# Kernel optimization log

Hardware: AMD Instinct MI355X
Metric: run time of the kernel (lower is better)

Reference implementation:

```python
import jax, jax.numpy as jnp
import numpy as np

B, S, E = 4, 2048, 1024
H, D = 16, 64  # num_heads, head_size; H*D == E


def setup_inputs() -> dict:
    key = jax.random.key(0)
    ks = jax.random.split(key, 6)
    scale = E ** -0.5
    x = jax.random.normal(ks[0], (B, S, E), dtype=jnp.float32)
    # per-head bias-free q/k/v projections, stacked over heads: [H, E, D]
    Wq = jax.random.normal(ks[1], (H, E, D), dtype=jnp.float32) * scale
    Wk = jax.random.normal(ks[2], (H, E, D), dtype=jnp.float32) * scale
    Wv = jax.random.normal(ks[3], (H, E, D), dtype=jnp.float32) * scale
    # output projection: Linear(H*D, E) with bias
    Wproj = jax.random.normal(ks[4], (H * D, E), dtype=jnp.float32) * ((H * D) ** -0.5)
    bproj = jax.random.normal(ks[5], (E,), dtype=jnp.float32) * 0.01
    return {"x": x, "Wq": Wq, "Wk": Wk, "Wv": Wv, "Wproj": Wproj, "bproj": bproj}


def reference(x, Wq, Wk, Wv, Wproj, bproj):
    # Batched equivalent of the per-head loop: each head h computes
    # q = x @ Wq[h], k = x @ Wk[h], v = x @ Wv[h]
    q = jnp.einsum("bse,hed->bhsd", x, Wq)
    k = jnp.einsum("bse,hed->bhsd", x, Wk)
    v = jnp.einsum("bse,hed->bhsd", x, Wv)
    # causal scaled dot-product attention, scale = head_size**-0.5
    scores = jnp.einsum("bhqd,bhkd->bhqk", q, k) * (D ** -0.5)
    causal = jnp.tril(jnp.ones((S, S), dtype=bool))  # [S, S]
    scores = jnp.where(causal, scores, jnp.finfo(scores.dtype).min)
    attn = jax.nn.softmax(scores, axis=-1)  # dropout = identity in eval
    out = jnp.einsum("bhqk,bhkd->bhqd", attn, v)
    # concat heads along the feature dim, then project (dropout = identity)
    out = out.transpose(0, 2, 1, 3).reshape(B, S, H * D)
    return out @ Wproj + bproj
```

## Files before the change

kernel.cpp:

```cpp
#include <hip/hip_runtime.h>
#include <stdint.h>

typedef unsigned short u16;
typedef __attribute__((ext_vector_type(8))) short bf16x8;
typedef __attribute__((ext_vector_type(8))) unsigned short u16x8;
typedef __attribute__((ext_vector_type(4))) float f32x4;

#define S_LEN 2048
#define EDIM 1024
#define NH 16
#define HD 64

static __device__ __forceinline__ u16 f2bf(float f) {
  union { float f; uint32_t u; } v; v.f = f;
  uint32_t r = v.u + 0x7fffu + ((v.u >> 16) & 1u);
  return (u16)(r >> 16);
}

static __device__ __forceinline__ void gload_lds16(const u16* g, u16* l) {
  __builtin_amdgcn_global_load_lds(
      (const __attribute__((address_space(1))) void*)g,
      (__attribute__((address_space(3))) void*)l, 16, 0, 0);
}

static __device__ __forceinline__ bf16x8 gload16(const u16* p) {
  bf16x8 r;
  asm volatile("global_load_dwordx4 %0, %1, off" : "=v"(r) : "v"(p));
  return r;
}

#define WAIT_VM(n)                                   \
  do {                                               \
    asm volatile("s_waitcnt vmcnt(" #n ")");         \
    __builtin_amdgcn_sched_barrier(0);               \
  } while (0)

#define BARRIER()                                    \
  do {                                               \
    __builtin_amdgcn_s_barrier();                    \
    __builtin_amdgcn_sched_barrier(0);               \
  } while (0)

__global__ __launch_bounds__(256) void pack_inputs(
    const float* __restrict__ x, const float* __restrict__ Wq,
    const float* __restrict__ Wk, const float* __restrict__ Wv,
    const float* __restrict__ Wp,
    u16* __restrict__ xb, u16* __restrict__ wqkvT, u16* __restrict__ wprojT) {
  const int blk = blockIdx.x;
  const int tid = threadIdx.x;
  if (blk < 8192) {
    int idx = blk * 256 + tid;
    float4 v = ((const float4*)x)[idx];
    ushort4 o;
    o.x = f2bf(v.x); o.y = f2bf(v.y); o.z = f2bf(v.z); o.w = f2bf(v.w);
    ((ushort4*)xb)[idx] = o;
    return;
  }
  __shared__ u16 tile[64][65];
  const float* src;
  size_t src_rs;
  u16* dst;
  if (blk < 8960) {
    int t = blk - 8192;
    int mh = t >> 4;
    int et = t & 15;
    int m = mh >> 4, h = mh & 15;
    const float* W = (m == 0) ? Wq : (m == 1) ? Wk : Wv;
    src = W + ((size_t)(h * EDIM + et * 64)) * HD;
    src_rs = HD;
    dst = wqkvT + (size_t)(m * 1024 + h * 64) * 1024 + et * 64;
  } else {
    int t = blk - 8960;
    int kt = t >> 4, nt = t & 15;
    src = Wp + (size_t)(kt * 64) * 1024 + nt * 64;
    src_rs = 1024;
    dst = wprojT + (size_t)(nt * 64) * 1024 + kt * 64;
  }
  {
    const int rr = tid >> 4;
    const int c4 = (tid & 15) << 2;
#pragma unroll
    for (int p = 0; p < 4; p++) {
      const int r = p * 16 + rr;
      float4 v = *(const float4*)(src + (size_t)r * src_rs + c4);
      tile[r][c4 + 0] = f2bf(v.x);
      tile[r][c4 + 1] = f2bf(v.y);
      tile[r][c4 + 2] = f2bf(v.z);
      tile[r][c4 + 3] = f2bf(v.w);
    }
  }
  __syncthreads();
  {
    const int rr = tid >> 3;
    const int c8 = (tid & 7) << 3;
#pragma unroll
    for (int p = 0; p < 2; p++) {
      const int r = p * 32 + rr;
      u16x8 o;
#pragma unroll
      for (int j = 0; j < 8; j++) o[j] = tile[c8 + j][r];
      *(u16x8*)(dst + (size_t)r * 1024 + c8) = o;
    }
  }
}

template <int EPI>
__global__ __launch_bounds__(256) void gemm128(
    const u16* __restrict__ A, const u16* __restrict__ Bt,
    const float* __restrict__ bias,
    u16* __restrict__ o0, u16* __restrict__ o1, u16* __restrict__ o2,
    float* __restrict__ of, int K, int N) {
  __shared__ __align__(16) u16 As[128 * 64];
  __shared__ __align__(16) u16 Bs[128 * 64];
  const int tid  = threadIdx.x;
  const int lane = tid & 63;
  const int wave = tid >> 6;
  const int wm = wave >> 1;
  const int wn = wave & 1;
  const int col = lane & 15;
  const int quad = lane >> 4;
  const int cs = col & 7;
  const int m0 = blockIdx.y << 7;
  const int n0 = blockIdx.x << 7;

  const int srow  = lane >> 3;
  const int sslot = (lane & 7) ^ srow;
  const u16* gA = A + (size_t)(m0 + (wave << 5) + srow) * K + sslot * 8;
  const u16* gB = Bt + (size_t)(n0 + (wave << 5) + srow) * K + sslot * 8;
  u16* lA = &As[(wave << 5) << 6];
  u16* lB = &Bs[(wave << 5) << 6];

  f32x4 acc[4][4];
#pragma unroll
  for (int i = 0; i < 4; i++)
#pragma unroll
    for (int j = 0; j < 4; j++) acc[i][j] = (f32x4){0.f, 0.f, 0.f, 0.f};

  for (int kk = 0; kk < K; kk += 64) {
    __syncthreads();
#pragma unroll
    for (int i = 0; i < 4; i++) {
      gload_lds16(gA + (size_t)(i * 8) * K + kk, lA + i * 512);
      gload_lds16(gB + (size_t)(i * 8) * K + kk, lB + i * 512);
    }
    __syncthreads();

#pragma unroll
    for (int x = 0; x < 2; x++) {
      bf16x8 af[4], bfr[4];
#pragma unroll
      for (int i = 0; i < 4; i++)
        af[i] = *(const bf16x8*)(
            &As[((wm * 64 + i * 16 + col) << 6) + ((((x << 2) + quad) ^ cs) << 3)]);
#pragma unroll
      for (int j = 0; j < 4; j++)
        bfr[j] = *(const bf16x8*)(
            &Bs[((wn * 64 + j * 16 + col) << 6) + ((((x << 2) + quad) ^ cs) << 3)]);
#pragma unroll
      for (int i = 0; i < 4; i++)
#pragma unroll
        for (int j = 0; j < 4; j++)
          acc[i][j] = __builtin_amdgcn_mfma_f32_16x16x32_bf16(af[i], bfr[j],
                                                              acc[i][j], 0, 0, 0);
    }
  }

#pragma unroll
  for (int i = 0; i < 4; i++) {
#pragma unroll
    for (int j = 0; j < 4; j++) {
      const int rg0 = m0 + wm * 64 + i * 16 + quad * 4;
      const int cg = n0 + wn * 64 + j * 16 + col;
      if (EPI == 0) {
        const int mat = cg >> 10;
        const int rem = cg & 1023;
        const int h = rem >> 6;
        const int d = rem & 63;
        const int b = rg0 >> 11;
        const int s0 = rg0 & 2047;
        if (mat == 2) {
          ushort4 o;
          o.x = f2bf(acc[i][j][0]); o.y = f2bf(acc[i][j][1]);
          o.z = f2bf(acc[i][j][2]); o.w = f2bf(acc[i][j][3]);
          *(ushort4*)(&o2[(((size_t)(b * NH + h) * HD + d) << 11) + s0]) = o;
        } else {
          u16* dst = (mat == 0) ? o0 : o1;
#pragma unroll
          for (int r = 0; r < 4; r++)
            dst[((size_t)((b * NH + h) * S_LEN + s0 + r) << 6) + d] =
                f2bf(acc[i][j][r]);
        }
      } else {
#pragma unroll
        for (int r = 0; r < 4; r++)
          of[(size_t)(rg0 + r) * N + cg] = acc[i][j][r] + bias[cg];
      }
    }
  }
}

__global__ __launch_bounds__(256, 3) void attn_fused(
    const u16* __restrict__ Q, const u16* __restrict__ K,
    const u16* __restrict__ Vt, u16* __restrict__ O) {
  __shared__ __align__(16) u16 Kbuf[2][64 * 64];
  __shared__ __align__(16) u16 Vbuf[2][64 * 64];
  __shared__ __align__(16) u16 Ps[4][2][16 * 72];

  const int tid  = threadIdx.x;
  const int lane = tid & 63;
  const int wave = tid >> 6;
  const int col  = lane & 15;
  const int quad = lane >> 4;
  const int gid  = blockIdx.x;
  const int bh = ((gid & 7) << 3) | ((gid >> 3) & 7);
  const int qb = 15 - (gid >> 6);
  const int b = bh >> 4;
  const int h = bh & 15;
  const int q0w = qb * 128 + wave * 32;

  const u16* Kbh = K + (size_t)bh * S_LEN * HD;
  const u16* Vbh = Vt + (size_t)bh * HD * S_LEN;

  const int srow  = lane >> 3;
  const int sslot = (lane & 7) ^ srow;
  const int r0a = wave * 16;
  const int r0b = wave * 16 + 8;

  const float C1 = 0.125f * 1.44269504f;
  const float C2 = 8.0f * 1.44269504f;

  bf16x8 qf[2][2];
#pragma unroll
  for (int a = 0; a < 2; a++) {
    const u16* Qrow = Q + ((size_t)bh * S_LEN + q0w + a * 16 + col) * HD;
    qf[a][0] = gload16(Qrow + quad * 8);
    qf[a][1] = gload16(Qrow + 32 + quad * 8);
  }

  f32x4 oacc[2][4];
#pragma unroll
  for (int a = 0; a < 2; a++)
#pragma unroll
    for (int n = 0; n < 4; n++) oacc[a][n] = (f32x4){0.f, 0.f, 0.f, 0.f};
  float lrow[2][4] = {{0.f, 0.f, 0.f, 0.f}, {0.f, 0.f, 0.f, 0.f}};

  auto STAGE = [&](int buf, int kv0) {
    gload_lds16(Kbh + (size_t)(kv0 + r0a + srow) * HD + sslot * 8,
                &Kbuf[buf][r0a * 64]);
    gload_lds16(Kbh + (size_t)(kv0 + r0b + srow) * HD + sslot * 8,
                &Kbuf[buf][r0b * 64]);
    gload_lds16(Vbh + (size_t)(r0a + srow) * S_LEN + kv0 + sslot * 8,
                &Vbuf[buf][r0a * 64]);
    gload_lds16(Vbh + (size_t)(r0b + srow) * S_LEN + kv0 + sslot * 8,
                &Vbuf[buf][r0b * 64]);
  };

  const int T = 2 * qb + 2;
  int cur = 0;
  STAGE(0, 0);
  WAIT_VM(0);
  BARRIER();

  for (int t = 0; t < T; t++) {
    const int kv0 = t << 6;
    if (t + 1 < T) STAGE(cur ^ 1, kv0 + 64);

    if (kv0 <= q0w + 31) {
      f32x4 sc[2][4];
#pragma unroll
      for (int j = 0; j < 4; j++) {
        const u16* kr = &Kbuf[cur][(j * 16 + col) * 64];
        const bf16x8 kf0 = *(const bf16x8*)(kr + ((quad ^ (col & 7)) << 3));
        const bf16x8 kf1 = *(const bf16x8*)(kr + (((4 + quad) ^ (col & 7)) << 3));
#pragma unroll
        for (int a = 0; a < 2; a++) {
          sc[a][j] = (f32x4){0.f, 0.f, 0.f, 0.f};
          sc[a][j] = __builtin_amdgcn_mfma_f32_16x16x32_bf16(qf[a][0], kf0, sc[a][j], 0, 0, 0);
          sc[a][j] = __builtin_amdgcn_mfma_f32_16x16x32_bf16(qf[a][1], kf1, sc[a][j], 0, 0, 0);
        }
      }

      if (kv0 + 63 > q0w) {
#pragma unroll
        for (int a = 0; a < 2; a++)
#pragma unroll
          for (int r = 0; r < 4; r++) {
            const int ql = q0w - kv0 + a * 16 + quad * 4 + r;
#pragma unroll
            for (int j = 0; j < 4; j++) {
              float p = exp2f(sc[a][j][r] * C1 - C2);
              if (j * 16 + col > ql) p = 0.f;
              lrow[a][r] += p;
              Ps[wave][a][(quad * 4 + r) * 72 + j * 16 + col] = f2bf(p);
            }
          }
      } else {
#pragma unroll
        for (int a = 0; a < 2; a++)
#pragma unroll
          for (int r = 0; r < 4; r++)
#pragma unroll
            for (int j = 0; j < 4; j++) {
              const float p = exp2f(sc[a][j][r] * C1 - C2);
              lrow[a][r] += p;
              Ps[wave][a][(quad * 4 + r) * 72 + j * 16 + col] = f2bf(p);
            }
      }
      bf16x8 pf[2][2];
#pragma unroll
      for (int a = 0; a < 2; a++) {
        pf[a][0] = *(const bf16x8*)(&Ps[wave][a][col * 72 + quad * 8]);
        pf[a][1] = *(const bf16x8*)(&Ps[wave][a][col * 72 + 32 + quad * 8]);
      }

#pragma unroll
      for (int n = 0; n < 4; n++) {
        const u16* vr = &Vbuf[cur][(n * 16 + col) * 64];
        const bf16x8 vf0 = *(const bf16x8*)(vr + ((quad ^ (col & 7)) << 3));
        const bf16x8 vf1 = *(const bf16x8*)(vr + (((4 + quad) ^ (col & 7)) << 3));
#pragma unroll
        for (int a = 0; a < 2; a++) {
          oacc[a][n] = __builtin_amdgcn_mfma_f32_16x16x32_bf16(pf[a][0], vf0, oacc[a][n], 0, 0, 0);
          oacc[a][n] = __builtin_amdgcn_mfma_f32_16x16x32_bf16(pf[a][1], vf1, oacc[a][n], 0, 0, 0);
        }
      }
    }

    WAIT_VM(0);
    BARRIER();
    cur ^= 1;
  }

#pragma unroll
  for (int a = 0; a < 2; a++)
#pragma unroll
    for (int r = 0; r < 4; r++) {
      float l = lrow[a][r];
#pragma unroll
      for (int off = 1; off < 16; off <<= 1) l += __shfl_xor(l, off);
      const float inv = 1.0f / l;
      const size_t row = (size_t)b * S_LEN + q0w + a * 16 + quad * 4 + r;
#pragma unroll
      for (int n = 0; n < 4; n++)
        O[row * EDIM + h * HD + n * 16 + col] = f2bf(oacc[a][n][r] * inv);
    }
}

extern "C" void kernel_launch(void* const* d_in, const int* in_sizes, int n_in,
                              void* d_out, int out_size, void* d_ws, size_t ws_size,
                              hipStream_t stream) {
  const float* x  = (const float*)d_in[0];
  const float* Wq = (const float*)d_in[1];
  const float* Wk = (const float*)d_in[2];
  const float* Wv = (const float*)d_in[3];
  const float* Wp = (const float*)d_in[4];
  const float* bp = (const float*)d_in[5];
  float* out = (float*)d_out;

  char* ws = (char*)d_ws;
  u16* wqkvT  = (u16*)(ws);
  u16* wprojT = (u16*)(ws + 6291456);
  u16* Qb     = (u16*)(ws + 8388608);
  u16* Kb     = (u16*)(ws + 25165824);
  u16* Vtb    = (u16*)(ws + 41943040);
  u16* xb     = (u16*)(ws + 58720256);
  u16* Ob     = xb;

  pack_inputs<<<dim3(9216), dim3(256), 0, stream>>>(x, Wq, Wk, Wv, Wp,
                                                    xb, wqkvT, wprojT);
  gemm128<0><<<dim3(24, 64), dim3(256), 0, stream>>>(
      xb, wqkvT, (const float*)nullptr, Qb, Kb, Vtb, (float*)nullptr, 1024, 3072);
  attn_fused<<<dim3(1024), dim3(256), 0, stream>>>(Qb, Kb, Vtb, Ob);
  gemm128<1><<<dim3(8, 64), dim3(256), 0, stream>>>(
      Ob, wprojT, bp, (u16*)nullptr, (u16*)nullptr, (u16*)nullptr, out, 1024, 1024);
}
```

Before: 261.8 us.

## Compute transposed attention scores to keep P in registers via shuffles instead of LDS

```diff
diff --git a/kernel.cpp b/kernel.cpp
--- a/kernel.cpp
+++ b/kernel.cpp
@@ -15,6 +15,12 @@
   union { float f; uint32_t u; } v; v.f = f;
   uint32_t r = v.u + 0x7fffu + ((v.u >> 16) & 1u);
   return (u16)(r >> 16);
+}
+
+static __device__ __forceinline__ uint32_t cvtpk_bf16(float a, float b) {
+  uint32_t r;
+  asm("v_cvt_pk_bf16_f32 %0, %1, %2" : "=v"(r) : "v"(a), "v"(b));
+  return r;
 }
 
 static __device__ __forceinline__ void gload_lds16(const u16* g, u16* l) {
@@ -199,18 +205,18 @@
   }
 }
 
-__global__ __launch_bounds__(256, 3) void attn_fused(
+__global__ __launch_bounds__(256, 4) void attn_fused(
     const u16* __restrict__ Q, const u16* __restrict__ K,
     const u16* __restrict__ Vt, u16* __restrict__ O) {
   __shared__ __align__(16) u16 Kbuf[2][64 * 64];
   __shared__ __align__(16) u16 Vbuf[2][64 * 64];
-  __shared__ __align__(16) u16 Ps[4][2][16 * 72];
 
   const int tid  = threadIdx.x;
   const int lane = tid & 63;
   const int wave = tid >> 6;
   const int col  = lane & 15;
   const int quad = lane >> 4;
+  const int cs   = col & 7;
   const int gid  = blockIdx.x;
   const int bh = ((gid & 7) << 3) | ((gid >> 3) & 7);
   const int qb = 15 - (gid >> 6);
@@ -221,6 +227,10 @@
   const u16* Kbh = K + (size_t)bh * S_LEN * HD;
   const u16* Vbh = Vt + (size_t)bh * HD * S_LEN;
 
+  const int s0lane = col + ((quad & 1) << 5);
+  const int s1lane = s0lane + 16;
+  const bool hi_j = quad >= 2;
+
   const int srow  = lane >> 3;
   const int sslot = (lane & 7) ^ srow;
   const int r0a = wave * 16;
@@ -242,7 +252,7 @@
   for (int a = 0; a < 2; a++)
 #pragma unroll
     for (int n = 0; n < 4; n++) oacc[a][n] = (f32x4){0.f, 0.f, 0.f, 0.f};
-  float lrow[2][4] = {{0.f, 0.f, 0.f, 0.f}, {0.f, 0.f, 0.f, 0.f}};
+  float lacc[2] = {0.f, 0.f};
 
   auto STAGE = [&](int buf, int kv0) {
     gload_lds16(Kbh + (size_t)(kv0 + r0a + srow) * HD + sslot * 8,
@@ -266,62 +276,72 @@
     if (t + 1 < T) STAGE(cur ^ 1, kv0 + 64);
 
     if (kv0 <= q0w + 31) {
-      f32x4 sc[2][4];
+      f32x4 ssc[2][4];
 #pragma unroll
       for (int j = 0; j < 4; j++) {
         const u16* kr = &Kbuf[cur][(j * 16 + col) * 64];
-        const bf16x8 kf0 = *(const bf16x8*)(kr + ((quad ^ (col & 7)) << 3));
-        const bf16x8 kf1 = *(const bf16x8*)(kr + (((4 + quad) ^ (col & 7)) << 3));
+        const bf16x8 kf0 = *(const bf16x8*)(kr + ((quad ^ cs) << 3));
+        const bf16x8 kf1 = *(const bf16x8*)(kr + (((4 + quad) ^ cs) << 3));
 #pragma unroll
         for (int a = 0; a < 2; a++) {
-          sc[a][j] = (f32x4){0.f, 0.f, 0.f, 0.f};
-          sc[a][j] = __builtin_amdgcn_mfma_f32_16x16x32_bf16(qf[a][0], kf0, sc[a][j], 0, 0, 0);
-          sc[a][j] = __builtin_amdgcn_mfma_f32_16x16x32_bf16(qf[a][1], kf1, sc[a][j], 0, 0, 0);
+          ssc[a][j] = (f32x4){0.f, 0.f, 0.f, 0.f};
+          ssc[a][j] = __builtin_amdgcn_mfma_f32_16x16x32_bf16(kf0, qf[a][0], ssc[a][j], 0, 0, 0);
+          ssc[a][j] = __builtin_amdgcn_mfma_f32_16x16x32_bf16(kf1, qf[a][1], ssc[a][j], 0, 0, 0);
         }
       }
 
-      if (kv0 + 63 > q0w) {
-#pragma unroll
-        for (int a = 0; a < 2; a++)
+      uint32_t pk[2][4][2];
+      const bool diag = (kv0 + 63 > q0w);
+#pragma unroll
+      for (int a = 0; a < 2; a++) {
+#pragma unroll
+        for (int j = 0; j < 4; j++) {
+          float p[4];
 #pragma unroll
           for (int r = 0; r < 4; r++) {
-            const int ql = q0w - kv0 + a * 16 + quad * 4 + r;
-#pragma unroll
-            for (int j = 0; j < 4; j++) {
-              float p = exp2f(sc[a][j][r] * C1 - C2);
-              if (j * 16 + col > ql) p = 0.f;
-              lrow[a][r] += p;
-              Ps[wave][a][(quad * 4 + r) * 72 + j * 16 + col] = f2bf(p);
+            float v = exp2f(ssc[a][j][r] * C1 - C2);
+            if (diag) {
+              const int kl = j * 16 + quad * 4 + r;
+              const int ql = q0w - kv0 + a * 16 + col;
+              if (kl > ql) v = 0.f;
             }
+            p[r] = v;
           }
-      } else {
-#pragma unroll
-        for (int a = 0; a < 2; a++)
-#pragma unroll
-          for (int r = 0; r < 4; r++)
-#pragma unroll
-            for (int j = 0; j < 4; j++) {
-              const float p = exp2f(sc[a][j][r] * C1 - C2);
-              lrow[a][r] += p;
-              Ps[wave][a][(quad * 4 + r) * 72 + j * 16 + col] = f2bf(p);
-            }
+          lacc[a] += (p[0] + p[1]) + (p[2] + p[3]);
+          pk[a][j][0] = cvtpk_bf16(p[0], p[1]);
+          pk[a][j][1] = cvtpk_bf16(p[2], p[3]);
+        }
       }
-      bf16x8 pf[2][2];
-#pragma unroll
-      for (int a = 0; a < 2; a++) {
-        pf[a][0] = *(const bf16x8*)(&Ps[wave][a][col * 72 + quad * 8]);
-        pf[a][1] = *(const bf16x8*)(&Ps[wave][a][col * 72 + 32 + quad * 8]);
-      }
-
-#pragma unroll
-      for (int n = 0; n < 4; n++) {
-        const u16* vr = &Vbuf[cur][(n * 16 + col) * 64];
-        const bf16x8 vf0 = *(const bf16x8*)(vr + ((quad ^ (col & 7)) << 3));
-        const bf16x8 vf1 = *(const bf16x8*)(vr + (((4 + quad) ^ (col & 7)) << 3));
+
+#pragma unroll
+      for (int kb = 0; kb < 2; kb++) {
+        bf16x8 pfrag[2];
 #pragma unroll
         for (int a = 0; a < 2; a++) {
-          oacc[a][n] = __builtin_amdgcn_mfma_f32_16x16x32_bf16(pf[a][0], vf0, oacc[a][n], 0, 0, 0);
-          oacc[a][n] = __builtin_amdgcn_mfma_f32_16x16x32_bf16(pf[a][1], vf1, oacc[a][n], 0, 0, 0);
+          const uint32_t tL0 = __shfl((int)pk[a][2 * kb][0], s0lane);
+          const uint32_t tH0 = __shfl((int)pk[a][2 * kb + 1][0], s0lane);
+          const uint32_t tL1 = __shfl((int)pk[a][2 * kb][1], s0lane);
+          const uint32_t tH1 = __shfl((int)pk[a][2 * kb + 1][1], s0lane);
+          const uint32_t tL2 = __shfl((int)pk[a][2 * kb][0], s1lane);
+          const uint32_t tH2 = __shfl((int)pk[a][2 * kb + 1][0], s1lane);
+          const uint32_t tL3 = __shfl((int)pk[a][2 * kb][1], s1lane);
+          const uint32_t tH3 = __shfl((int)pk[a][2 * kb + 1][1], s1lane);
+          union { uint32_t u[4]; bf16x8 v; } U;
+          U.u[0] = hi_j ? tH0 : tL0;
+          U.u[1] = hi_j ? tH1 : tL1;
+          U.u[2] = hi_j ? tH2 : tL2;
+          U.u[3] = hi_j ? tH3 : tL3;
+          pfrag[a] = U.v;
+        }
+#pragma unroll
+        for (int n = 0; n < 4; n++) {
+          const u16* vr = &Vbuf[cur][(n * 16 + col) * 64];
+          const bf16x8 vfk =
+              *(const bf16x8*)(vr + ((((kb << 2) + quad) ^ cs) << 3));
+#pragma unroll
+          for (int a = 0; a < 2; a++)
+            oacc[a][n] = __builtin_amdgcn_mfma_f32_16x16x32_bf16(
+                vfk, pfrag[a], oacc[a][n], 0, 0, 0);
         }
       }
     }
@@ -332,18 +352,22 @@
   }
 
 #pragma unroll
-  for (int a = 0; a < 2; a++)
-#pragma unroll
-    for (int r = 0; r < 4; r++) {
-      float l = lrow[a][r];
-#pragma unroll
-      for (int off = 1; off < 16; off <<= 1) l += __shfl_xor(l, off);
-      const float inv = 1.0f / l;
-      const size_t row = (size_t)b * S_LEN + q0w + a * 16 + quad * 4 + r;
-#pragma unroll
-      for (int n = 0; n < 4; n++)
-        O[row * EDIM + h * HD + n * 16 + col] = f2bf(oacc[a][n][r] * inv);
-    }
+  for (int a = 0; a < 2; a++) {
+    float l = lacc[a];
+    l += __shfl_xor(l, 16);
+    l += __shfl_xor(l, 32);
+    const float inv = 1.0f / l;
+    const size_t qrow = (size_t)b * S_LEN + q0w + a * 16 + col;
+#pragma unroll
+    for (int n = 0; n < 4; n++) {
+      ushort4 o;
+      o.x = f2bf(oacc[a][n][0] * inv);
+      o.y = f2bf(oacc[a][n][1] * inv);
+      o.z = f2bf(oacc[a][n][2] * inv);
+      o.w = f2bf(oacc[a][n][3] * inv);
+      *(ushort4*)(&O[qrow * EDIM + h * HD + n * 16 + quad * 4]) = o;
+    }
+  }
 }
 
 extern "C" void kernel_launch(void* const* d_in, const int* in_sizes, int n_in,
```

New measurement: 264.9 us. Within noise of the previous version (+1.2%).

## Widen attention blocks to 8 waves and fold softmax scale into Wq

Applied to the files above, without the earlier changes.

```diff
diff --git a/kernel.cpp b/kernel.cpp
--- a/kernel.cpp
+++ b/kernel.cpp
@@ -15,6 +15,12 @@
   union { float f; uint32_t u; } v; v.f = f;
   uint32_t r = v.u + 0x7fffu + ((v.u >> 16) & 1u);
   return (u16)(r >> 16);
+}
+
+static __device__ __forceinline__ uint32_t cvtpk_bf16(float a, float b) {
+  uint32_t r;
+  asm("v_cvt_pk_bf16_f32 %0, %1, %2" : "=v"(r) : "v"(a), "v"(b));
+  return r;
 }
 
 static __device__ __forceinline__ void gload_lds16(const u16* g, u16* l) {
@@ -60,12 +66,14 @@
   const float* src;
   size_t src_rs;
   u16* dst;
+  float wscale = 1.0f;
   if (blk < 8960) {
     int t = blk - 8192;
     int mh = t >> 4;
     int et = t & 15;
     int m = mh >> 4, h = mh & 15;
     const float* W = (m == 0) ? Wq : (m == 1) ? Wk : Wv;
+    if (m == 0) wscale = 0.1803368801111204f;
     src = W + ((size_t)(h * EDIM + et * 64)) * HD;
     src_rs = HD;
     dst = wqkvT + (size_t)(m * 1024 + h * 64) * 1024 + et * 64;
@@ -83,10 +91,10 @@
     for (int p = 0; p < 4; p++) {
       const int r = p * 16 + rr;
       float4 v = *(const float4*)(src + (size_t)r * src_rs + c4);
-      tile[r][c4 + 0] = f2bf(v.x);
-      tile[r][c4 + 1] = f2bf(v.y);
-      tile[r][c4 + 2] = f2bf(v.z);
-      tile[r][c4 + 3] = f2bf(v.w);
+      tile[r][c4 + 0] = f2bf(v.x * wscale);
+      tile[r][c4 + 1] = f2bf(v.y * wscale);
+      tile[r][c4 + 2] = f2bf(v.z * wscale);
+      tile[r][c4 + 3] = f2bf(v.w * wscale);
     }
   }
   __syncthreads();
@@ -199,35 +207,33 @@
   }
 }
 
-__global__ __launch_bounds__(256, 3) void attn_fused(
+__global__ __launch_bounds__(512, 4) void attn_fused(
     const u16* __restrict__ Q, const u16* __restrict__ K,
     const u16* __restrict__ Vt, u16* __restrict__ O) {
   __shared__ __align__(16) u16 Kbuf[2][64 * 64];
   __shared__ __align__(16) u16 Vbuf[2][64 * 64];
-  __shared__ __align__(16) u16 Ps[4][2][16 * 72];
+  __shared__ __align__(16) u16 Ps[8][16 * 72];
 
   const int tid  = threadIdx.x;
   const int lane = tid & 63;
   const int wave = tid >> 6;
   const int col  = lane & 15;
   const int quad = lane >> 4;
+  const int cs   = col & 7;
   const int gid  = blockIdx.x;
   const int bh = ((gid & 7) << 3) | ((gid >> 3) & 7);
-  const int qb = 15 - (gid >> 6);
+  const int hi = gid >> 6;
+  const int qb = (hi < 4) ? (7 - hi) : (hi - 4);
   const int b = bh >> 4;
   const int h = bh & 15;
-  const int q0w = qb * 128 + wave * 32;
+  const int q0w = qb * 256 + wave * 32;
 
   const u16* Kbh = K + (size_t)bh * S_LEN * HD;
   const u16* Vbh = Vt + (size_t)bh * HD * S_LEN;
 
   const int srow  = lane >> 3;
   const int sslot = (lane & 7) ^ srow;
-  const int r0a = wave * 16;
-  const int r0b = wave * 16 + 8;
-
-  const float C1 = 0.125f * 1.44269504f;
-  const float C2 = 8.0f * 1.44269504f;
+  const int r0 = wave * 8;
 
   bf16x8 qf[2][2];
 #pragma unroll
@@ -245,17 +251,13 @@
   float lrow[2][4] = {{0.f, 0.f, 0.f, 0.f}, {0.f, 0.f, 0.f, 0.f}};
 
   auto STAGE = [&](int buf, int kv0) {
-    gload_lds16(Kbh + (size_t)(kv0 + r0a + srow) * HD + sslot * 8,
-                &Kbuf[buf][r0a * 64]);
-    gload_lds16(Kbh + (size_t)(kv0 + r0b + srow) * HD + sslot * 8,
-                &Kbuf[buf][r0b * 64]);
-    gload_lds16(Vbh + (size_t)(r0a + srow) * S_LEN + kv0 + sslot * 8,
-                &Vbuf[buf][r0a * 64]);
-    gload_lds16(Vbh + (size_t)(r0b + srow) * S_LEN + kv0 + sslot * 8,
-                &Vbuf[buf][r0b * 64]);
+    gload_lds16(Kbh + (size_t)(kv0 + r0 + srow) * HD + sslot * 8,
+                &Kbuf[buf][r0 * 64]);
+    gload_lds16(Vbh + (size_t)(r0 + srow) * S_LEN + kv0 + sslot * 8,
+                &Vbuf[buf][r0 * 64]);
   };
 
-  const int T = 2 * qb + 2;
+  const int T = 4 * qb + 4;
   int cur = 0;
   STAGE(0, 0);
   WAIT_VM(0);
@@ -270,8 +272,8 @@
 #pragma unroll
       for (int j = 0; j < 4; j++) {
         const u16* kr = &Kbuf[cur][(j * 16 + col) * 64];
-        const bf16x8 kf0 = *(const bf16x8*)(kr + ((quad ^ (col & 7)) << 3));
-        const bf16x8 kf1 = *(const bf16x8*)(kr + (((4 + quad) ^ (col & 7)) << 3));
+        const bf16x8 kf0 = *(const bf16x8*)(kr + ((quad ^ cs) << 3));
+        const bf16x8 kf1 = *(const bf16x8*)(kr + (((4 + quad) ^ cs) << 3));
 #pragma unroll
         for (int a = 0; a < 2; a++) {
           sc[a][j] = (f32x4){0.f, 0.f, 0.f, 0.f};
@@ -280,48 +282,39 @@
         }
       }
 
-      if (kv0 + 63 > q0w) {
-#pragma unroll
-        for (int a = 0; a < 2; a++)
-#pragma unroll
-          for (int r = 0; r < 4; r++) {
-            const int ql = q0w - kv0 + a * 16 + quad * 4 + r;
-#pragma unroll
-            for (int j = 0; j < 4; j++) {
-              float p = exp2f(sc[a][j][r] * C1 - C2);
-              if (j * 16 + col > ql) p = 0.f;
-              lrow[a][r] += p;
-              Ps[wave][a][(quad * 4 + r) * 72 + j * 16 + col] = f2bf(p);
+      const bool diag = (kv0 + 63 > q0w);
+#pragma unroll
+      for (int a = 0; a < 2; a++) {
+#pragma unroll
+        for (int r = 0; r < 4; r++) {
+          float p[4];
+#pragma unroll
+          for (int j = 0; j < 4; j++) {
+            float v = exp2f(sc[a][j][r]);
+            if (diag) {
+              const int ql = q0w - kv0 + a * 16 + quad * 4 + r;
+              if (j * 16 + col > ql) v = 0.f;
             }
+            lrow[a][r] += v;
+            p[j] = v;
           }
-      } else {
-#pragma unroll
-        for (int a = 0; a < 2; a++)
-#pragma unroll
-          for (int r = 0; r < 4; r++)
-#pragma unroll
-            for (int j = 0; j < 4; j++) {
-              const float p = exp2f(sc[a][j][r] * C1 - C2);
-              lrow[a][r] += p;
-              Ps[wave][a][(quad * 4 + r) * 72 + j * 16 + col] = f2bf(p);
-            }
-      }
-      bf16x8 pf[2][2];
-#pragma unroll
-      for (int a = 0; a < 2; a++) {
-        pf[a][0] = *(const bf16x8*)(&Ps[wave][a][col * 72 + quad * 8]);
-        pf[a][1] = *(const bf16x8*)(&Ps[wave][a][col * 72 + 32 + quad * 8]);
-      }
-
-#pragma unroll
-      for (int n = 0; n < 4; n++) {
-        const u16* vr = &Vbuf[cur][(n * 16 + col) * 64];
-        const bf16x8 vf0 = *(const bf16x8*)(vr + ((quad ^ (col & 7)) << 3));
-        const bf16x8 vf1 = *(const bf16x8*)(vr + (((4 + quad) ^ (col & 7)) << 3));
-#pragma unroll
-        for (int a = 0; a < 2; a++) {
-          oacc[a][n] = __builtin_amdgcn_mfma_f32_16x16x32_bf16(pf[a][0], vf0, oacc[a][n], 0, 0, 0);
-          oacc[a][n] = __builtin_amdgcn_mfma_f32_16x16x32_bf16(pf[a][1], vf1, oacc[a][n], 0, 0, 0);
+          const uint32_t pk0 = cvtpk_bf16(p[0], p[1]);
+          const uint32_t pk1 = cvtpk_bf16(p[2], p[3]);
+          u16* row = &Ps[wave][(quad * 4 + r) * 72 + col];
+          row[0]  = (u16)pk0;
+          row[16] = (u16)(pk0 >> 16);
+          row[32] = (u16)pk1;
+          row[48] = (u16)(pk1 >> 16);
+        }
+        const bf16x8 pf0 = *(const bf16x8*)(&Ps[wave][col * 72 + quad * 8]);
+        const bf16x8 pf1 = *(const bf16x8*)(&Ps[wave][col * 72 + 32 + quad * 8]);
+#pragma unroll
+        for (int n = 0; n < 4; n++) {
+          const u16* vr = &Vbuf[cur][(n * 16 + col) * 64];
+          const bf16x8 vf0 = *(const bf16x8*)(vr + ((quad ^ cs) << 3));
+          const bf16x8 vf1 = *(const bf16x8*)(vr + (((4 + quad) ^ cs) << 3));
+          oacc[a][n] = __builtin_amdgcn_mfma_f32_16x16x32_bf16(pf0, vf0, oacc[a][n], 0, 0, 0);
+          oacc[a][n] = __builtin_amdgcn_mfma_f32_16x16x32_bf16(pf1, vf1, oacc[a][n], 0, 0, 0);
         }
       }
     }
@@ -370,7 +363,7 @@
                                                     xb, wqkvT, wprojT);
   gemm128<0><<<dim3(24, 64), dim3(256), 0, stream>>>(
       xb, wqkvT, (const float*)nullptr, Qb, Kb, Vtb, (float*)nullptr, 1024, 3072);
-  attn_fused<<<dim3(1024), dim3(256), 0, stream>>>(Qb, Kb, Vtb, Ob);
+  attn_fused<<<dim3(512), dim3(512), 0, stream>>>(Qb, Kb, Vtb, Ob);
   gemm128<1><<<dim3(8, 64), dim3(256), 0, stream>>>(
       Ob, wprojT, bp, (u16*)nullptr, (u16*)nullptr, (u16*)nullptr, out, 1024, 1024);
 }
```

Result: slower. 275.5 us (+5.2%).
